# Kernel optimization log

Measured on AMD Instinct MI355X. Metric: run time of the kernel, lower is better.

## Reference

```python
import jax, jax.numpy as jnp
import numpy as np

B, S, D, H, DK, DV = 4, 2048, 512, 8, 64, 64


def setup_inputs() -> dict:
    key0 = jax.random.key(0)
    ks = jax.random.split(key0, 11)
    w = 0.02
    return {
        "query": jax.random.normal(ks[0], (B, S, D), dtype=jnp.float32),
        "key": jax.random.normal(ks[1], (B, S, D), dtype=jnp.float32),
        "value": jax.random.normal(ks[2], (B, S, D), dtype=jnp.float32),
        "Wq": jax.random.normal(ks[3], (D, DK), dtype=jnp.float32) * w,
        "bq": jnp.zeros((DK,), dtype=jnp.float32),
        "Wk": jax.random.normal(ks[4], (D, DK), dtype=jnp.float32) * w,
        "bk": jnp.zeros((DK,), dtype=jnp.float32),
        "Wv": jax.random.normal(ks[5], (D, DV), dtype=jnp.float32) * w,
        "bv": jnp.zeros((DV,), dtype=jnp.float32),
        "Wo": jax.random.normal(ks[6], (H * DV, D), dtype=jnp.float32) * w,
        "bo": jnp.zeros((D,), dtype=jnp.float32),
    }


def reference(query, key, value, Wq, bq, Wk, bk, Wv, bv, Wo, bo):
    # NOTE: original module applies the SAME Dense layers to every head
    # (q_list = [self.query(query) for _ in range(heads)]), so all H heads
    # are mathematically identical -> compute one head and replicate.
    # NOTE: V is projected from `key`, not `value` (faithful to source bug).
    q = query @ Wq + bq          # [B, S, DK]
    k = key @ Wk + bk            # [B, S, DK]
    v = key @ Wv + bv            # [B, S, DV]
    scale = np.sqrt(DK).astype(np.float32)
    scores = jnp.einsum("bqd,bkd->bqk", q, k) / scale  # [B, S, S]
    # masked_mha=True and training=True -> causal mask, fill -1e19
    causal = jnp.triu(jnp.ones((S, S), dtype=scores.dtype), 1)
    scores = scores + causal * jnp.asarray(-1e19, scores.dtype)
    attn = jax.nn.softmax(scores, axis=-1)              # [B, S, S]
    o = jnp.einsum("bqk,bkv->bqv", attn, v)             # [B, S, DV]
    # concat of H identical heads along last axis == tile
    concat = jnp.tile(o, (1, 1, H))                     # [B, S, H*DV]
    return concat @ Wo + bo                             # [B, S, D]
```

## Files before the change

kernel.cpp:

```cpp
#include <hip/hip_runtime.h>
#include <hip/hip_bf16.h>


#define BB 4
#define SS 2048
#define BS (BB*SS)
#define MSHIFT 8.0f
#define NCH 8

typedef __bf16 v8bf __attribute__((ext_vector_type(8)));
typedef __bf16 v4bf __attribute__((ext_vector_type(4)));
typedef float  v4f  __attribute__((ext_vector_type(4)));

__device__ inline v8bf cvt8(float4 f0, float4 f1) {
    v8bf r;
    r[0] = (__bf16)f0.x; r[1] = (__bf16)f0.y; r[2] = (__bf16)f0.z; r[3] = (__bf16)f0.w;
    r[4] = (__bf16)f1.x; r[5] = (__bf16)f1.y; r[6] = (__bf16)f1.z; r[7] = (__bf16)f1.w;
    return r;
}

__global__ __launch_bounds__(256) void projprep_kernel(
    const float* __restrict__ query, const float* __restrict__ key,
    const float* __restrict__ Wq, const float* __restrict__ bq,
    const float* __restrict__ Wk, const float* __restrict__ bk,
    const float* __restrict__ Wv, const float* __restrict__ bv,
    const float* __restrict__ Wo,
    __bf16* __restrict__ Qp, __bf16* __restrict__ Kp, __bf16* __restrict__ Vt,
    __bf16* __restrict__ WoEt)
{
    __shared__ __bf16 Ws[2][16][520];
    const int t  = threadIdx.x;
    const int vb = blockIdx.x;

    if (vb >= 1024) {
        const int k = vb - 1024;
        for (int d = t; d < 512; d += 256) {
            float sum = 0.f;
#pragma unroll
            for (int h = 0; h < 8; h++) sum += Wo[(size_t)(h * 64 + k) * 512 + d];
            WoEt[d * 64 + k] = (__bf16)sum;
        }
        return;
    }

    const int lane = t & 63, w = t >> 6, lq = lane & 15, quad = lane >> 4;
    const int kind = vb >> 9;
    const int v2   = vb & 511;
    const int cb   = (v2 & 3) * 16;
    const int rows = (v2 >> 2) * 64 + w * 16;
    const float qscale = 0.125f * 1.44269504088896340736f;

    {
        const int c4 = (t & 3) * 4;
        const int kk = t >> 2;
        if (kind == 0) {
#pragma unroll
            for (int pass = 0; pass < 8; pass++) {
                int k = kk + pass * 64;
                float4 f = *(const float4*)(Wq + (size_t)k * 64 + cb + c4);
                Ws[0][c4 + 0][k] = (__bf16)(f.x * qscale);
                Ws[0][c4 + 1][k] = (__bf16)(f.y * qscale);
                Ws[0][c4 + 2][k] = (__bf16)(f.z * qscale);
                Ws[0][c4 + 3][k] = (__bf16)(f.w * qscale);
            }
        } else {
#pragma unroll
            for (int pass = 0; pass < 8; pass++) {
                int k = kk + pass * 64;
                float4 fk = *(const float4*)(Wk + (size_t)k * 64 + cb + c4);
                float4 fv = *(const float4*)(Wv + (size_t)k * 64 + cb + c4);
                Ws[0][c4 + 0][k] = (__bf16)fk.x;
                Ws[0][c4 + 1][k] = (__bf16)fk.y;
                Ws[0][c4 + 2][k] = (__bf16)fk.z;
                Ws[0][c4 + 3][k] = (__bf16)fk.w;
                Ws[1][c4 + 0][k] = (__bf16)fv.x;
                Ws[1][c4 + 1][k] = (__bf16)fv.y;
                Ws[1][c4 + 2][k] = (__bf16)fv.z;
                Ws[1][c4 + 3][k] = (__bf16)fv.w;
            }
        }
    }
    __syncthreads();

    const float* arow = ((kind == 0) ? query : key) + (size_t)(rows + lq) * 512;

    if (kind == 0) {
        const float bb = bq[cb + lq] * qscale;
        v4f acc = {bb, bb, bb, bb};
#pragma unroll 4
        for (int k0 = 0; k0 < 512; k0 += 32) {
            float4 f0 = *(const float4*)(arow + k0 + quad * 8);
            float4 f1 = *(const float4*)(arow + k0 + quad * 8 + 4);
            v8bf a = cvt8(f0, f1);
            v8bf b = *(const v8bf*)&Ws[0][lq][k0 + quad * 8];
            acc = __builtin_amdgcn_mfma_f32_16x16x32_bf16(a, b, acc, 0, 0, 0);
        }
#pragma unroll
        for (int r = 0; r < 4; r++)
            Qp[(size_t)(rows + quad * 4 + r) * 64 + cb + lq] = (__bf16)acc[r];
    } else {
        const float bk_ = bk[cb + lq], bv_ = bv[cb + lq];
        v4f ak = {bk_, bk_, bk_, bk_}, av = {bv_, bv_, bv_, bv_};
#pragma unroll 4
        for (int k0 = 0; k0 < 512; k0 += 32) {
            float4 f0 = *(const float4*)(arow + k0 + quad * 8);
            float4 f1 = *(const float4*)(arow + k0 + quad * 8 + 4);
            v8bf a  = cvt8(f0, f1);
            v8bf b0 = *(const v8bf*)&Ws[0][lq][k0 + quad * 8];
            v8bf b1 = *(const v8bf*)&Ws[1][lq][k0 + quad * 8];
            ak = __builtin_amdgcn_mfma_f32_16x16x32_bf16(a, b0, ak, 0, 0, 0);
            av = __builtin_amdgcn_mfma_f32_16x16x32_bf16(a, b1, av, 0, 0, 0);
        }
#pragma unroll
        for (int r = 0; r < 4; r++)
            Kp[(size_t)(rows + quad * 4 + r) * 64 + cb + lq] = (__bf16)ak[r];
        v4bf o4; o4[0] = (__bf16)av[0]; o4[1] = (__bf16)av[1];
        o4[2] = (__bf16)av[2]; o4[3] = (__bf16)av[3];
        *(v4bf*)&Vt[(size_t)(cb + lq) * BS + rows + quad * 4] = o4;
    }
}

__global__ __launch_bounds__(256) void attn_kernel(
    const __bf16* __restrict__ Qp,
    const __bf16* __restrict__ Kp,
    const __bf16* __restrict__ Vt,
    __bf16* __restrict__ Opart,
    float* __restrict__ lpart,
    const __bf16* __restrict__ WoEt,
    const float* __restrict__ bo,
    float* __restrict__ out,
    unsigned* __restrict__ cnt)
{
    __shared__ __bf16 Ks[64][72];
    __shared__ __bf16 Vs[64][72];
    __shared__ __bf16 Ps[4][16][72];
    __shared__ unsigned arr_s;

    const int t    = threadIdx.x;
    const int lane = t & 63;
    const int w    = t >> 6;
    const int b    = blockIdx.x & 3;
    const int qt   = 31 - (blockIdx.x >> 2);
    const int c    = blockIdx.y;
    const int qbase = qt * 64;
    const int L    = qbase + 64;
    const int cs   = ((L + NCH * 64 - 1) / (NCH * 64)) * 64;
    const int klo  = c * cs;
    const int khi  = min(klo + cs, L);
    const size_t bbase = (size_t)b * SS;

    const int lq   = lane & 15;
    const int quad = lane >> 4;
    const int qrow_w = qbase + w * 16;
    const int wmax   = qrow_w + 15;

    const size_t qoff = (bbase + qrow_w + lq) * 64;
    v8bf qa0 = *(const v8bf*)(Qp + qoff + quad * 8);
    v8bf qa1 = *(const v8bf*)(Qp + qoff + 32 + quad * 8);

    v8bf ones;
#pragma unroll
    for (int i = 0; i < 8; i++) ones[i] = (__bf16)1.0f;

    v4f o[4] = {};
    v4f lacc = {};

    const int ky0 = t >> 3,         dd0 = (t & 7) * 8;
    const int ky1 = (t + 256) >> 3, dd1 = dd0;

    v8bf kpre0, kpre1, vpre0, vpre1;
    if (klo < khi) {
        kpre0 = *(const v8bf*)(Kp + (bbase + klo + ky0) * 64 + dd0);
        kpre1 = *(const v8bf*)(Kp + (bbase + klo + ky1) * 64 + dd1);
        vpre0 = *(const v8bf*)(Vt + (size_t)ky0 * BS + bbase + klo + dd0);
        vpre1 = *(const v8bf*)(Vt + (size_t)ky1 * BS + bbase + klo + dd1);
    }

    for (int kb = klo; kb < khi; kb += 64) {
        __syncthreads();
        *(v8bf*)&Ks[ky0][dd0] = kpre0;
        *(v8bf*)&Ks[ky1][dd1] = kpre1;
        *(v8bf*)&Vs[ky0][dd0] = vpre0;
        *(v8bf*)&Vs[ky1][dd1] = vpre1;
        if (kb + 64 < khi) {
            kpre0 = *(const v8bf*)(Kp + (bbase + kb + 64 + ky0) * 64 + dd0);
            kpre1 = *(const v8bf*)(Kp + (bbase + kb + 64 + ky1) * 64 + dd1);
            vpre0 = *(const v8bf*)(Vt + (size_t)ky0 * BS + bbase + kb + 64 + dd0);
            vpre1 = *(const v8bf*)(Vt + (size_t)ky1 * BS + bbase + kb + 64 + dd1);
        }
        __syncthreads();
        if (kb > wmax) continue;

        v4f s[4];
#pragma unroll
        for (int n = 0; n < 4; n++) {
            v8bf ka  = *(const v8bf*)&Ks[n * 16 + lq][quad * 8];
            v8bf kb2 = *(const v8bf*)&Ks[n * 16 + lq][32 + quad * 8];
            v4f z = {0.f, 0.f, 0.f, 0.f};
            z    = __builtin_amdgcn_mfma_f32_16x16x32_bf16(qa0, ka,  z, 0, 0, 0);
            s[n] = __builtin_amdgcn_mfma_f32_16x16x32_bf16(qa1, kb2, z, 0, 0, 0);
        }

        const int row0 = qrow_w + quad * 4;
        const int col0 = kb + lq;
#pragma unroll
        for (int n = 0; n < 4; n++)
#pragma unroll
            for (int r = 0; r < 4; r++) {
                float e = exp2f(s[n][r] - MSHIFT);
                e = (col0 + n * 16 > row0 + r) ? 0.f : e;
                Ps[w][quad * 4 + r][n * 16 + lq] = (__bf16)e;
            }
        v8bf pa0 = *(const v8bf*)&Ps[w][lq][quad * 8];
        v8bf pa1 = *(const v8bf*)&Ps[w][lq][32 + quad * 8];

        lacc = __builtin_amdgcn_mfma_f32_16x16x32_bf16(pa0, ones, lacc, 0, 0, 0);
        lacc = __builtin_amdgcn_mfma_f32_16x16x32_bf16(pa1, ones, lacc, 0, 0, 0);

#pragma unroll
        for (int vt2 = 0; vt2 < 4; vt2++) {
            v8bf vb0 = *(const v8bf*)&Vs[vt2 * 16 + lq][quad * 8];
            v8bf vb1 = *(const v8bf*)&Vs[vt2 * 16 + lq][32 + quad * 8];
            o[vt2] = __builtin_amdgcn_mfma_f32_16x16x32_bf16(pa0, vb0, o[vt2], 0, 0, 0);
            o[vt2] = __builtin_amdgcn_mfma_f32_16x16x32_bf16(pa1, vb1, o[vt2], 0, 0, 0);
        }
    }

#pragma unroll
    for (int vt2 = 0; vt2 < 4; vt2++)
#pragma unroll
        for (int r = 0; r < 4; r++) {
            int qrow = qrow_w + quad * 4 + r;
            Opart[((size_t)c * BS + bbase + qrow) * 64 + vt2 * 16 + lq] = (__bf16)o[vt2][r];
        }
    if (lq < 4) {
        int qrow = qrow_w + quad * 4 + lq;
        lpart[(size_t)c * BS + bbase + qrow] = lacc[lq];
    }

    __syncthreads();
    if (t == 0)
        arr_s = __hip_atomic_fetch_add(&cnt[b * 32 + qt], 1u,
                                       __ATOMIC_ACQ_REL, __HIP_MEMORY_SCOPE_AGENT);
    __syncthreads();
    if (arr_s != NCH - 1u) return;

    __bf16 (&Os)[64][72] = Ks;
    {
        const int row = t >> 2;
        const int d0  = (t & 3) * 16;
        const size_t grow = bbase + qbase + row;
        float den = 0.f;
#pragma unroll
        for (int c2 = 0; c2 < NCH; c2++) den += lpart[(size_t)c2 * BS + grow];
        const float inv = 1.f / den;
        float m[16] = {0.f, 0.f, 0.f, 0.f, 0.f, 0.f, 0.f, 0.f,
                       0.f, 0.f, 0.f, 0.f, 0.f, 0.f, 0.f, 0.f};
#pragma unroll
        for (int c2 = 0; c2 < NCH; c2++) {
            const __bf16* src = Opart + ((size_t)c2 * BS + grow) * 64 + d0;
            v8bf u0 = *(const v8bf*)src;
            v8bf u1 = *(const v8bf*)(src + 8);
#pragma unroll
            for (int j = 0; j < 8; j++) { m[j] += (float)u0[j]; m[8 + j] += (float)u1[j]; }
        }
#pragma unroll
        for (int j = 0; j < 16; j++) Os[row][d0 + j] = (__bf16)(m[j] * inv);
    }
    __syncthreads();

    {
        v8bf a0 = *(const v8bf*)&Os[w * 16 + lq][quad * 8];
        v8bf a1 = *(const v8bf*)&Os[w * 16 + lq][32 + quad * 8];
        const int orow = qbase + w * 16;
#pragma unroll 4
        for (int i = 0; i < 32; i++) {
            const int cb2 = i * 16;
            v8bf b0 = *(const v8bf*)(WoEt + (size_t)(cb2 + lq) * 64 + quad * 8);
            v8bf b1 = *(const v8bf*)(WoEt + (size_t)(cb2 + lq) * 64 + 32 + quad * 8);
            const float bb2 = bo[cb2 + lq];
            v4f acc = {bb2, bb2, bb2, bb2};
            acc = __builtin_amdgcn_mfma_f32_16x16x32_bf16(a0, b0, acc, 0, 0, 0);
            acc = __builtin_amdgcn_mfma_f32_16x16x32_bf16(a1, b1, acc, 0, 0, 0);
#pragma unroll
            for (int r = 0; r < 4; r++)
                out[(size_t)(bbase + orow + quad * 4 + r) * 512 + cb2 + lq] = acc[r];
        }
    }
}

extern "C" void kernel_launch(void* const* d_in, const int* in_sizes, int n_in,
                              void* d_out, int out_size, void* d_ws, size_t ws_size,
                              hipStream_t stream) {
    const float* query = (const float*)d_in[0];
    const float* key   = (const float*)d_in[1];
    const float* Wq = (const float*)d_in[3];
    const float* bq = (const float*)d_in[4];
    const float* Wk = (const float*)d_in[5];
    const float* bk = (const float*)d_in[6];
    const float* Wv = (const float*)d_in[7];
    const float* bv = (const float*)d_in[8];
    const float* Wo = (const float*)d_in[9];
    const float* bo = (const float*)d_in[10];
    float* out = (float*)d_out;

    char* p = (char*)d_ws;
    __bf16* Qp    = (__bf16*)p; p += (size_t)BS * 64 * 2;
    __bf16* Kp    = (__bf16*)p; p += (size_t)BS * 64 * 2;
    __bf16* Vtg   = (__bf16*)p; p += (size_t)BS * 64 * 2;
    __bf16* Opart = (__bf16*)p; p += (size_t)NCH * BS * 64 * 2;
    float* lpart = (float*)p;  p += (size_t)NCH * BS * 4;
    __bf16* WoEt = (__bf16*)p; p += (size_t)64 * 512 * 2;
    uintptr_t pa = ((uintptr_t)p + 255) & ~(uintptr_t)255;
    unsigned* cnt = (unsigned*)pa;

    (void)hipMemsetAsync(cnt, 0, 512, stream);
    projprep_kernel<<<1088, 256, 0, stream>>>(
        query, key, Wq, bq, Wk, bk, Wv, bv, Wo, Qp, Kp, Vtg, WoEt);
    attn_kernel<<<dim3(128, NCH), 256, 0, stream>>>(
        Qp, Kp, Vtg, Opart, lpart, WoEt, bo, out, cnt);
}
```

Baseline: 177.6 us.

## Remove split-K chunking and cross-block merge from attention kernel

Each block now processes the full causal key range for its 64-row query tile, instead of splitting keys across 8 chunks that are merged by the last-arriving block through atomics. This drops the partial-output buffers, the atomic counter, the memset and the merge pass. In exchange, the grid shrinks to 128 blocks with very unbalanced work across query tiles, which reduces parallelism on a GPU with many CUs.

```diff
diff --git a/kernel.cpp b/kernel.cpp
--- a/kernel.cpp
+++ b/kernel.cpp
@@ -6,7 +6,6 @@
 #define SS 2048
 #define BS (BB*SS)
 #define MSHIFT 8.0f
-#define NCH 8
 
 typedef __bf16 v8bf __attribute__((ext_vector_type(8)));
 typedef __bf16 v4bf __attribute__((ext_vector_type(4)));
@@ -124,35 +123,26 @@
     const __bf16* __restrict__ Qp,
     const __bf16* __restrict__ Kp,
     const __bf16* __restrict__ Vt,
-    __bf16* __restrict__ Opart,
-    float* __restrict__ lpart,
     const __bf16* __restrict__ WoEt,
     const float* __restrict__ bo,
-    float* __restrict__ out,
-    unsigned* __restrict__ cnt)
+    float* __restrict__ out)
 {
     __shared__ __bf16 Ks[64][72];
     __shared__ __bf16 Vs[64][72];
     __shared__ __bf16 Ps[4][16][72];
-    __shared__ unsigned arr_s;
 
     const int t    = threadIdx.x;
     const int lane = t & 63;
     const int w    = t >> 6;
     const int b    = blockIdx.x & 3;
-    const int qt   = 31 - (blockIdx.x >> 2);
-    const int c    = blockIdx.y;
+    const int qt   = blockIdx.x >> 2;
     const int qbase = qt * 64;
     const int L    = qbase + 64;
-    const int cs   = ((L + NCH * 64 - 1) / (NCH * 64)) * 64;
-    const int klo  = c * cs;
-    const int khi  = min(klo + cs, L);
     const size_t bbase = (size_t)b * SS;
 
     const int lq   = lane & 15;
     const int quad = lane >> 4;
     const int qrow_w = qbase + w * 16;
-    const int wmax   = qrow_w + 15;
 
     const size_t qoff = (bbase + qrow_w + lq) * 64;
     v8bf qa0 = *(const v8bf*)(Qp + qoff + quad * 8);
@@ -168,28 +158,24 @@
     const int ky0 = t >> 3,         dd0 = (t & 7) * 8;
     const int ky1 = (t + 256) >> 3, dd1 = dd0;
 
-    v8bf kpre0, kpre1, vpre0, vpre1;
-    if (klo < khi) {
-        kpre0 = *(const v8bf*)(Kp + (bbase + klo + ky0) * 64 + dd0);
-        kpre1 = *(const v8bf*)(Kp + (bbase + klo + ky1) * 64 + dd1);
-        vpre0 = *(const v8bf*)(Vt + (size_t)ky0 * BS + bbase + klo + dd0);
-        vpre1 = *(const v8bf*)(Vt + (size_t)ky1 * BS + bbase + klo + dd1);
-    }
-
-    for (int kb = klo; kb < khi; kb += 64) {
+    v8bf kpre0 = *(const v8bf*)(Kp + (bbase + ky0) * 64 + dd0);
+    v8bf kpre1 = *(const v8bf*)(Kp + (bbase + ky1) * 64 + dd1);
+    v8bf vpre0 = *(const v8bf*)(Vt + (size_t)ky0 * BS + bbase + dd0);
+    v8bf vpre1 = *(const v8bf*)(Vt + (size_t)ky1 * BS + bbase + dd1);
+
+    for (int kb = 0; kb < L; kb += 64) {
         __syncthreads();
         *(v8bf*)&Ks[ky0][dd0] = kpre0;
         *(v8bf*)&Ks[ky1][dd1] = kpre1;
         *(v8bf*)&Vs[ky0][dd0] = vpre0;
         *(v8bf*)&Vs[ky1][dd1] = vpre1;
-        if (kb + 64 < khi) {
+        if (kb + 64 < L) {
             kpre0 = *(const v8bf*)(Kp + (bbase + kb + 64 + ky0) * 64 + dd0);
             kpre1 = *(const v8bf*)(Kp + (bbase + kb + 64 + ky1) * 64 + dd1);
             vpre0 = *(const v8bf*)(Vt + (size_t)ky0 * BS + bbase + kb + 64 + dd0);
             vpre1 = *(const v8bf*)(Vt + (size_t)ky1 * BS + bbase + kb + 64 + dd1);
         }
         __syncthreads();
-        if (kb > wmax) continue;
 
         v4f s[4];
 #pragma unroll
@@ -226,53 +212,21 @@
         }
     }
 
-#pragma unroll
-    for (int vt2 = 0; vt2 < 4; vt2++)
-#pragma unroll
-        for (int r = 0; r < 4; r++) {
-            int qrow = qrow_w + quad * 4 + r;
-            Opart[((size_t)c * BS + bbase + qrow) * 64 + vt2 * 16 + lq] = (__bf16)o[vt2][r];
-        }
-    if (lq < 4) {
-        int qrow = qrow_w + quad * 4 + lq;
-        lpart[(size_t)c * BS + bbase + qrow] = lacc[lq];
-    }
-
     __syncthreads();
-    if (t == 0)
-        arr_s = __hip_atomic_fetch_add(&cnt[b * 32 + qt], 1u,
-                                       __ATOMIC_ACQ_REL, __HIP_MEMORY_SCOPE_AGENT);
-    __syncthreads();
-    if (arr_s != NCH - 1u) return;
-
     __bf16 (&Os)[64][72] = Ks;
-    {
-        const int row = t >> 2;
-        const int d0  = (t & 3) * 16;
-        const size_t grow = bbase + qbase + row;
-        float den = 0.f;
-#pragma unroll
-        for (int c2 = 0; c2 < NCH; c2++) den += lpart[(size_t)c2 * BS + grow];
-        const float inv = 1.f / den;
-        float m[16] = {0.f, 0.f, 0.f, 0.f, 0.f, 0.f, 0.f, 0.f,
-                       0.f, 0.f, 0.f, 0.f, 0.f, 0.f, 0.f, 0.f};
-#pragma unroll
-        for (int c2 = 0; c2 < NCH; c2++) {
-            const __bf16* src = Opart + ((size_t)c2 * BS + grow) * 64 + d0;
-            v8bf u0 = *(const v8bf*)src;
-            v8bf u1 = *(const v8bf*)(src + 8);
-#pragma unroll
-            for (int j = 0; j < 8; j++) { m[j] += (float)u0[j]; m[8 + j] += (float)u1[j]; }
-        }
-#pragma unroll
-        for (int j = 0; j < 16; j++) Os[row][d0 + j] = (__bf16)(m[j] * inv);
+#pragma unroll
+    for (int r = 0; r < 4; r++) {
+        const float inv = 1.f / lacc[r];
+#pragma unroll
+        for (int vt2 = 0; vt2 < 4; vt2++)
+            Os[w * 16 + quad * 4 + r][vt2 * 16 + lq] = (__bf16)(o[vt2][r] * inv);
     }
     __syncthreads();
 
     {
         v8bf a0 = *(const v8bf*)&Os[w * 16 + lq][quad * 8];
         v8bf a1 = *(const v8bf*)&Os[w * 16 + lq][32 + quad * 8];
-        const int orow = qbase + w * 16;
+        const size_t orow = bbase + qbase + w * 16;
 #pragma unroll 4
         for (int i = 0; i < 32; i++) {
             const int cb2 = i * 16;
@@ -284,7 +238,7 @@
             acc = __builtin_amdgcn_mfma_f32_16x16x32_bf16(a1, b1, acc, 0, 0, 0);
 #pragma unroll
             for (int r = 0; r < 4; r++)
-                out[(size_t)(bbase + orow + quad * 4 + r) * 512 + cb2 + lq] = acc[r];
+                out[(orow + quad * 4 + r) * 512 + cb2 + lq] = acc[r];
         }
     }
 }
@@ -305,18 +259,12 @@
     float* out = (float*)d_out;
 
     char* p = (char*)d_ws;
-    __bf16* Qp    = (__bf16*)p; p += (size_t)BS * 64 * 2;
-    __bf16* Kp    = (__bf16*)p; p += (size_t)BS * 64 * 2;
-    __bf16* Vtg   = (__bf16*)p; p += (size_t)BS * 64 * 2;
-    __bf16* Opart = (__bf16*)p; p += (size_t)NCH * BS * 64 * 2;
-    float* lpart = (float*)p;  p += (size_t)NCH * BS * 4;
+    __bf16* Qp   = (__bf16*)p; p += (size_t)BS * 64 * 2;
+    __bf16* Kp   = (__bf16*)p; p += (size_t)BS * 64 * 2;
+    __bf16* Vtg  = (__bf16*)p; p += (size_t)BS * 64 * 2;
     __bf16* WoEt = (__bf16*)p; p += (size_t)64 * 512 * 2;
-    uintptr_t pa = ((uintptr_t)p + 255) & ~(uintptr_t)255;
-    unsigned* cnt = (unsigned*)pa;
-
-    (void)hipMemsetAsync(cnt, 0, 512, stream);
+
     projprep_kernel<<<1088, 256, 0, stream>>>(
         query, key, Wq, bq, Wk, bk, Wv, bv, Wo, Qp, Kp, Vtg, WoEt);
-    attn_kernel<<<dim3(128, NCH), 256, 0, stream>>>(
-        Qp, Kp, Vtg, Opart, lpart, WoEt, bo, out, cnt);
-}
+    attn_kernel<<<128, 256, 0, stream>>>(Qp, Kp, Vtg, WoEt, bo, out);
+}
```

Measured after the change: 162.5 us. -8.5%, faster.
